# Kernel optimization log

Hardware: AMD Instinct MI355X
Metric: run time of the kernel (lower is better)

Reference implementation:

```python
import jax, jax.numpy as jnp
import numpy as np

TOP_K = 4  # num_experts_per_tok


def setup_inputs() -> dict:
    key = jax.random.key(0)
    ks = jax.random.split(key, 5)
    T, H, M, E = 2048, 1024, 512, 32
    sH = 1.0 / np.sqrt(H)
    sM = 1.0 / np.sqrt(M)
    return {
        "x": jax.random.normal(ks[0], (T, 1, H), dtype=jnp.float32),
        "gate_w": jax.random.normal(ks[1], (E, H), dtype=jnp.float32) * sH,   # router nn.Linear weight [E, H]
        "w_gate": jax.random.normal(ks[2], (E, M, H), dtype=jnp.float32) * sH,  # ffn_gate_exps, per expert [M, H]
        "w_up": jax.random.normal(ks[3], (E, M, H), dtype=jnp.float32) * sH,    # ffn_up_exps
        "w_down": jax.random.normal(ks[4], (E, H, M), dtype=jnp.float32) * sM,  # ffn_down_exps, per expert [H, M]
    }


def reference(x, gate_w, w_gate, w_up, w_down):
    # x: [T, S, H]; only the last position is used (decode path)
    curr = x[:, -1, :]                                   # [T, H]
    T = curr.shape[0]
    E = gate_w.shape[0]

    # router: logits = curr @ gate_w^T, top-k, softmax over top-k logits
    logits = curr @ gate_w.T                             # [T, E]
    topk_vals, topk_ids = jax.lax.top_k(logits, TOP_K)   # [T, K]
    topk_weights = jax.nn.softmax(topk_vals, axis=-1)    # [T, K]

    # dense routing matrix [T, E]: weight for chosen experts, 0 elsewhere
    route = jnp.zeros((T, E), dtype=curr.dtype)
    route = route.at[jnp.arange(T)[:, None], topk_ids].add(topk_weights)

    # expert MLPs: gate/up -> silu(gate)*up -> down, weighted combine
    gate_act = jnp.einsum('th,emh->tem', curr, w_gate)   # [T, E, M]
    up_act = jnp.einsum('th,emh->tem', curr, w_up)
    mixed = jax.nn.silu(gate_act) * up_act * route[:, :, None]
    out = jnp.einsum('tem,ehm->th', mixed, w_down)       # [T, H]

    return out.reshape(T, 1, -1)
```

## Files before the change

kernel.cpp:

```cpp
#include <hip/hip_runtime.h>
#include <math.h>

#define T_TOK 2048
#define H_DIM 1024
#define M_DIM 512
#define E_NUM 32
#define TOPK  4

#define BT  128
#define BK  32
#define GU_BM 64
#define DN_BH 128
#define MAX_TILES 96

typedef __bf16 bf16x8 __attribute__((ext_vector_type(8)));
typedef float f32x4 __attribute__((ext_vector_type(4)));
typedef unsigned short u16x8 __attribute__((ext_vector_type(8)));

__device__ __forceinline__ unsigned short f2bf(float f) {
  unsigned u = __float_as_uint(f);
  return (unsigned short)((u + 0x7fffu + ((u >> 16) & 1u)) >> 16);
}
__device__ __forceinline__ float bf2f(unsigned short h) {
  return __uint_as_float(((unsigned)h) << 16);
}
__device__ __forceinline__ f32x4 mfma16(bf16x8 a, bf16x8 b, f32x4 c) {
  return __builtin_amdgcn_mfma_f32_16x16x32_bf16(a, b, c, 0, 0, 0);
}

__global__ __launch_bounds__(512) void split_x_kernel(
    const float* __restrict__ x, unsigned short* __restrict__ xh,
    unsigned short* __restrict__ xl) {
  int i = (blockIdx.x * 512 + threadIdx.x) * 8;
  float t8[8];
  *(float4*)t8 = *(const float4*)(x + i);
  *(float4*)(t8 + 4) = *(const float4*)(x + i + 4);
  u16x8 hv, lv;
  #pragma unroll
  for (int j = 0; j < 8; ++j) {
    unsigned short h = f2bf(t8[j]);
    hv[j] = h;
    lv[j] = f2bf(t8[j] - bf2f(h));
  }
  *(u16x8*)(xh + i) = hv;
  *(u16x8*)(xl + i) = lv;
}

__global__ __launch_bounds__(256) void gating_kernel(
    const float* __restrict__ x, const float* __restrict__ gate_w,
    int* __restrict__ topk_ids, float* __restrict__ topk_w) {
  __shared__ float xr[H_DIM];
  __shared__ float logits[E_NUM];
  int t = blockIdx.x;
  int tid = threadIdx.x;
  const float* xrow = x + (size_t)t * H_DIM;
  *(float4*)(xr + tid * 4) = *(const float4*)(xrow + tid * 4);
  __syncthreads();
  int wave = tid >> 6, lane = tid & 63;
  const float4* x4 = (const float4*)xr;
  for (int e8 = 0; e8 < 8; ++e8) {
    int e = wave * 8 + e8;
    const float4* g4 = (const float4*)(gate_w + (size_t)e * H_DIM);
    float p = 0.f;
    #pragma unroll
    for (int i = 0; i < 4; ++i) {
      float4 a = x4[lane + i * 64];
      float4 b = g4[lane + i * 64];
      p += a.x * b.x + a.y * b.y + a.z * b.z + a.w * b.w;
    }
    for (int off = 32; off > 0; off >>= 1) p += __shfl_down(p, off, 64);
    if (lane == 0) logits[e] = p;
  }
  __syncthreads();
  if (tid == 0) {
    float v[E_NUM];
    for (int e = 0; e < E_NUM; ++e) v[e] = logits[e];
    int ids[TOPK]; float vals[TOPK];
    for (int k = 0; k < TOPK; ++k) {
      int bi = 0; float bv = -1e30f;
      for (int e = 0; e < E_NUM; ++e) if (v[e] > bv) { bv = v[e]; bi = e; }
      ids[k] = bi; vals[k] = bv; v[bi] = -1e30f;
    }
    float m = vals[0];
    float w[TOPK]; float s = 0.f;
    for (int k = 0; k < TOPK; ++k) { w[k] = expf(vals[k] - m); s += w[k]; }
    float inv = 1.f / s;
    for (int k = 0; k < TOPK; ++k) {
      topk_ids[t * TOPK + k] = ids[k];
      topk_w[t * TOPK + k]   = w[k] * inv;
    }
  }
}

__global__ __launch_bounds__(256) void scatter_kernel(
    const int* __restrict__ topk_ids, int* __restrict__ cursors,
    int* __restrict__ tok_list) {
  int g = blockIdx.x * 256 + threadIdx.x;
  if (g >= T_TOK * TOPK) return;
  int e = topk_ids[g];
  int slot = atomicAdd(&cursors[e], 1);
  tok_list[e * T_TOK + slot] = g;
}

__global__ void build_tiles(const int* __restrict__ cursors,
                            int* __restrict__ n_tiles, int* __restrict__ tile_list) {
  int lane = threadIdx.x;
  int nt = 0;
  if (lane < E_NUM) nt = (cursors[lane] + BT - 1) / BT;
  int pfx = nt;
  for (int off = 1; off < 64; off <<= 1) {
    int v = __shfl_up(pfx, off, 64);
    if (lane >= off) pfx += v;
  }
  int excl = pfx - nt;
  if (lane == E_NUM - 1) *n_tiles = pfx;
  if (lane < E_NUM)
    for (int i = 0; i < nt; ++i) tile_list[excl + i] = (lane << 8) | i;
}

__global__ __launch_bounds__(512) void gateup_mfma(
    const unsigned short* __restrict__ xh, const unsigned short* __restrict__ xl,
    const float* __restrict__ w_gate, const float* __restrict__ w_up,
    const float* __restrict__ topk_w,
    const int* __restrict__ cursors, const int* __restrict__ tok_list,
    const int* __restrict__ n_tiles, const int* __restrict__ tile_list,
    unsigned short* __restrict__ mixed) {
  if (blockIdx.y >= *n_tiles) return;
  int tid = threadIdx.x;
  int entry = tile_list[blockIdx.y];
  int e = entry >> 8, tile = entry & 255;
  int cnt = cursors[e];
  int m0 = blockIdx.x * GU_BM;

  __shared__ unsigned short Ah[BT * BK], Al[BT * BK];
  __shared__ unsigned short Gh[GU_BM * BK], Uh[GU_BM * BK];
  __shared__ int   ent[BT];
  __shared__ float rw[BT];

  if (tid < BT) {
    int idx = tile * BT + tid;
    int en = (idx < cnt) ? tok_list[e * T_TOK + idx] : -1;
    ent[tid] = en;
    rw[tid]  = (en >= 0) ? topk_w[en] : 0.f;
  }
  __syncthreads();

  int arow = tid >> 2, akq = tid & 3;
  int aen = ent[arow];
  if (aen < 0) aen = ent[0];
  const unsigned short* pAh = xh + (size_t)(aen >> 2) * H_DIM + akq * 8;
  const unsigned short* pAl = xl + (size_t)(aen >> 2) * H_DIM + akq * 8;
  int aoff = (arow >> 4) * 512 + akq * 128 + (arow & 15) * 8;

  int bslot = tid & 255;
  int brow = bslot >> 2, bkq = bslot & 3;
  const float* pB = ((tid < 256) ? w_gate : w_up) +
                    ((size_t)e * M_DIM + m0 + brow) * H_DIM + bkq * 8;
  unsigned short* Bdst = (tid < 256) ? Gh : Uh;
  int boff = (brow >> 4) * 512 + bkq * 128 + (brow & 15) * 8;

  int lane = tid & 63, wid = tid >> 6;
  int wr = (wid >> 1) * 32;
  int wc = (wid & 1) * 32;
  int l16 = lane * 8;

  f32x4 accg[2][2] = {}; f32x4 accu[2][2] = {};

  u16x8 rah, ral; float bf8[8];
  rah = *(const u16x8*)pAh;
  ral = *(const u16x8*)pAl;
  *(float4*)bf8 = *(const float4*)pB;
  *(float4*)(bf8 + 4) = *(const float4*)(pB + 4);

  const int NK = H_DIM / BK;
  for (int ks = 0; ks < NK; ++ks) {
    u16x8 bh;
    #pragma unroll
    for (int j = 0; j < 8; ++j) bh[j] = f2bf(bf8[j]);
    __syncthreads();
    *(u16x8*)&Ah[aoff] = rah;
    *(u16x8*)&Al[aoff] = ral;
    *(u16x8*)&Bdst[boff] = bh;
    __syncthreads();
    if (ks + 1 < NK) {
      int kq = (ks + 1) * BK;
      rah = *(const u16x8*)(pAh + kq);
      ral = *(const u16x8*)(pAl + kq);
      *(float4*)bf8 = *(const float4*)(pB + kq);
      *(float4*)(bf8 + 4) = *(const float4*)(pB + kq + 4);
    }
    int ab = (wr >> 4) * 512 + l16;
    bf16x8 a0h = *(const bf16x8*)&Ah[ab];
    bf16x8 a1h = *(const bf16x8*)&Ah[ab + 512];
    bf16x8 a0l = *(const bf16x8*)&Al[ab];
    bf16x8 a1l = *(const bf16x8*)&Al[ab + 512];
    #pragma unroll
    for (int nf = 0; nf < 2; ++nf) {
      int nb = ((wc >> 4) + nf) * 512 + l16;
      bf16x8 g = *(const bf16x8*)&Gh[nb];
      bf16x8 u = *(const bf16x8*)&Uh[nb];
      accg[0][nf] = mfma16(a0h, g, accg[0][nf]);
      accg[0][nf] = mfma16(a0l, g, accg[0][nf]);
      accg[1][nf] = mfma16(a1h, g, accg[1][nf]);
      accg[1][nf] = mfma16(a1l, g, accg[1][nf]);
      accu[0][nf] = mfma16(a0h, u, accu[0][nf]);
      accu[0][nf] = mfma16(a0l, u, accu[0][nf]);
      accu[1][nf] = mfma16(a1h, u, accu[1][nf]);
      accu[1][nf] = mfma16(a1l, u, accu[1][nf]);
    }
  }

  #pragma unroll
  for (int mf = 0; mf < 2; ++mf) {
    #pragma unroll
    for (int j = 0; j < 4; ++j) {
      int tr = wr + mf * 16 + (lane >> 4) * 4 + j;
      int en = ent[tr];
      if (en < 0) continue;
      float w = rw[tr];
      #pragma unroll
      for (int nf = 0; nf < 2; ++nf) {
        float g = accg[mf][nf][j], u = accu[mf][nf][j];
        float val = (g / (1.f + __expf(-g))) * u * w;
        mixed[(size_t)en * M_DIM + m0 + wc + nf * 16 + (lane & 15)] = f2bf(val);
      }
    }
  }
}

__global__ __launch_bounds__(512) void down_mfma(
    const float* __restrict__ w_down, const unsigned short* __restrict__ mixed,
    const int* __restrict__ cursors, const int* __restrict__ tok_list,
    const int* __restrict__ n_tiles, const int* __restrict__ tile_list,
    float* __restrict__ out) {
  if (blockIdx.y >= *n_tiles) return;
  int tid = threadIdx.x;
  int entry = tile_list[blockIdx.y];
  int e = entry >> 8, tile = entry & 255;
  int cnt = cursors[e];
  int h0 = blockIdx.x * DN_BH;

  __shared__ unsigned short As[BT * BK];
  __shared__ unsigned short Bs[DN_BH * BK];
  __shared__ int ent[BT];

  if (tid < BT) {
    int idx = tile * BT + tid;
    ent[tid] = (idx < cnt) ? tok_list[e * T_TOK + idx] : -1;
  }
  __syncthreads();

  int arow = tid >> 2, akq = tid & 3;
  int aen = ent[arow];
  if (aen < 0) aen = ent[0];
  const unsigned short* pA = mixed + (size_t)aen * M_DIM + akq * 8;
  int aoff = (arow >> 4) * 512 + akq * 128 + (arow & 15) * 8;

  const float* pB = w_down + ((size_t)e * H_DIM + h0 + arow) * M_DIM + akq * 8;

  int lane = tid & 63, wid = tid >> 6;
  int wr = (wid >> 1) * 32, wc = (wid & 1) * 64;
  int l16 = lane * 8;

  f32x4 acc[2][4] = {};
  u16x8 ra; float bf8[8];
  ra = *(const u16x8*)pA;
  *(float4*)bf8 = *(const float4*)pB;
  *(float4*)(bf8 + 4) = *(const float4*)(pB + 4);

  const int NK = M_DIM / BK;
  for (int ks = 0; ks < NK; ++ks) {
    u16x8 bh;
    #pragma unroll
    for (int j = 0; j < 8; ++j) bh[j] = f2bf(bf8[j]);
    __syncthreads();
    *(u16x8*)&As[aoff] = ra;
    *(u16x8*)&Bs[aoff] = bh;
    __syncthreads();
    if (ks + 1 < NK) {
      int kq = (ks + 1) * BK;
      ra = *(const u16x8*)(pA + kq);
      *(float4*)bf8 = *(const float4*)(pB + kq);
      *(float4*)(bf8 + 4) = *(const float4*)(pB + kq + 4);
    }
    int ab = (wr >> 4) * 512 + l16;
    bf16x8 a0 = *(const bf16x8*)&As[ab];
    bf16x8 a1 = *(const bf16x8*)&As[ab + 512];
    #pragma unroll
    for (int nf = 0; nf < 4; ++nf) {
      bf16x8 b = *(const bf16x8*)&Bs[((wc >> 4) + nf) * 512 + l16];
      acc[0][nf] = mfma16(a0, b, acc[0][nf]);
      acc[1][nf] = mfma16(a1, b, acc[1][nf]);
    }
  }

  #pragma unroll
  for (int mf = 0; mf < 2; ++mf) {
    #pragma unroll
    for (int j = 0; j < 4; ++j) {
      int tr = wr + mf * 16 + (lane >> 4) * 4 + j;
      int en = ent[tr];
      if (en < 0) continue;
      int t = en >> 2;
      #pragma unroll
      for (int nf = 0; nf < 4; ++nf)
        atomicAdd(&out[(size_t)t * H_DIM + h0 + wc + nf * 16 + (lane & 15)],
                  acc[mf][nf][j]);
    }
  }
}

extern "C" void kernel_launch(void* const* d_in, const int* in_sizes, int n_in,
                              void* d_out, int out_size, void* d_ws, size_t ws_size,
                              hipStream_t stream) {
  const float* x      = (const float*)d_in[0];
  const float* gate_w = (const float*)d_in[1];
  const float* w_gate = (const float*)d_in[2];
  const float* w_up   = (const float*)d_in[3];
  const float* w_down = (const float*)d_in[4];
  float* out = (float*)d_out;

  char* ws = (char*)d_ws;
  size_t off = 0;
  int*   topk_ids  = (int*)(ws + off);   off += (size_t)T_TOK * TOPK * 4;
  float* topk_w    = (float*)(ws + off); off += (size_t)T_TOK * TOPK * 4;
  int*   cursors   = (int*)(ws + off);   off += 256;
  int*   n_tiles   = (int*)(ws + off);   off += 64;
  int*   tile_list = (int*)(ws + off);   off += MAX_TILES * 4 + 64;
  int*   tok_list  = (int*)(ws + off);   off += (size_t)E_NUM * T_TOK * 4;
  unsigned short* x_hi  = (unsigned short*)(ws + off); off += (size_t)T_TOK * H_DIM * 2;
  unsigned short* x_lo  = (unsigned short*)(ws + off); off += (size_t)T_TOK * H_DIM * 2;
  unsigned short* mixed = (unsigned short*)(ws + off); off += (size_t)T_TOK * TOPK * M_DIM * 2;

  hipMemsetAsync(cursors, 0, E_NUM * sizeof(int), stream);
  hipMemsetAsync(out, 0, (size_t)T_TOK * H_DIM * sizeof(float), stream);

  split_x_kernel<<<T_TOK * H_DIM / (512 * 8), 512, 0, stream>>>(x, x_hi, x_lo);
  gating_kernel<<<T_TOK, 256, 0, stream>>>(x, gate_w, topk_ids, topk_w);
  scatter_kernel<<<(T_TOK * TOPK) / 256, 256, 0, stream>>>(topk_ids, cursors, tok_list);
  build_tiles<<<1, 64, 0, stream>>>(cursors, n_tiles, tile_list);
  gateup_mfma<<<dim3(M_DIM / GU_BM, MAX_TILES), 512, 0, stream>>>(
      x_hi, x_lo, w_gate, w_up, topk_w, cursors, tok_list, n_tiles, tile_list, mixed);
  down_mfma<<<dim3(H_DIM / DN_BH, MAX_TILES), 512, 0, stream>>>(
      w_down, mixed, cursors, tok_list, n_tiles, tile_list, out);
}
```

Before: 163.1 us.

## Fuse split/scatter into gating, use global_load_lds with fp32 B tiles and smaller token tiles

After: 212.8 us. 30.4% more time.

```diff
diff --git a/kernel.cpp b/kernel.cpp
--- a/kernel.cpp
+++ b/kernel.cpp
@@ -7,15 +7,15 @@
 #define E_NUM 32
 #define TOPK  4
 
-#define BT  128
-#define BK  32
+#define BT    64
+#define BK    32
 #define GU_BM 64
 #define DN_BH 128
-#define MAX_TILES 96
+#define MAX_TILES 160
 
 typedef __bf16 bf16x8 __attribute__((ext_vector_type(8)));
 typedef float f32x4 __attribute__((ext_vector_type(4)));
-typedef unsigned short u16x8 __attribute__((ext_vector_type(8)));
+typedef unsigned short u16x4 __attribute__((ext_vector_type(4)));
 
 __device__ __forceinline__ unsigned short f2bf(float f) {
   unsigned u = __float_as_uint(f);
@@ -27,34 +27,42 @@
 __device__ __forceinline__ f32x4 mfma16(bf16x8 a, bf16x8 b, f32x4 c) {
   return __builtin_amdgcn_mfma_f32_16x16x32_bf16(a, b, c, 0, 0, 0);
 }
-
-__global__ __launch_bounds__(512) void split_x_kernel(
-    const float* __restrict__ x, unsigned short* __restrict__ xh,
-    unsigned short* __restrict__ xl) {
-  int i = (blockIdx.x * 512 + threadIdx.x) * 8;
-  float t8[8];
-  *(float4*)t8 = *(const float4*)(x + i);
-  *(float4*)(t8 + 4) = *(const float4*)(x + i + 4);
-  u16x8 hv, lv;
+__device__ __forceinline__ void gload16(const void* g, void* l) {
+  __builtin_amdgcn_global_load_lds(
+      (const __attribute__((address_space(1))) unsigned int*)g,
+      (__attribute__((address_space(3))) unsigned int*)l, 16, 0, 0);
+}
+__device__ __forceinline__ bf16x8 cvt8(f32x4 a, f32x4 b) {
+  bf16x8 r;
   #pragma unroll
-  for (int j = 0; j < 8; ++j) {
-    unsigned short h = f2bf(t8[j]);
-    hv[j] = h;
-    lv[j] = f2bf(t8[j] - bf2f(h));
-  }
-  *(u16x8*)(xh + i) = hv;
-  *(u16x8*)(xl + i) = lv;
+  for (int j = 0; j < 4; ++j) { r[j] = (__bf16)a[j]; r[4 + j] = (__bf16)b[j]; }
+  return r;
 }
 
 __global__ __launch_bounds__(256) void gating_kernel(
     const float* __restrict__ x, const float* __restrict__ gate_w,
-    int* __restrict__ topk_ids, float* __restrict__ topk_w) {
+    unsigned short* __restrict__ xh, unsigned short* __restrict__ xl,
+    float* __restrict__ topk_w, int* __restrict__ cursors,
+    int* __restrict__ tok_list) {
   __shared__ float xr[H_DIM];
   __shared__ float logits[E_NUM];
   int t = blockIdx.x;
   int tid = threadIdx.x;
   const float* xrow = x + (size_t)t * H_DIM;
-  *(float4*)(xr + tid * 4) = *(const float4*)(xrow + tid * 4);
+  float4 v = *(const float4*)(xrow + tid * 4);
+  *(float4*)(xr + tid * 4) = v;
+  {
+    float f[4] = {v.x, v.y, v.z, v.w};
+    u16x4 hv, lv;
+    #pragma unroll
+    for (int j = 0; j < 4; ++j) {
+      unsigned short h = f2bf(f[j]);
+      hv[j] = h;
+      lv[j] = f2bf(f[j] - bf2f(h));
+    }
+    *(u16x4*)(xh + (size_t)t * H_DIM + tid * 4) = hv;
+    *(u16x4*)(xl + (size_t)t * H_DIM + tid * 4) = lv;
+  }
   __syncthreads();
   int wave = tid >> 6, lane = tid & 63;
   const float4* x4 = (const float4*)xr;
@@ -73,33 +81,25 @@
   }
   __syncthreads();
   if (tid == 0) {
-    float v[E_NUM];
-    for (int e = 0; e < E_NUM; ++e) v[e] = logits[e];
+    float vv[E_NUM];
+    for (int e = 0; e < E_NUM; ++e) vv[e] = logits[e];
     int ids[TOPK]; float vals[TOPK];
     for (int k = 0; k < TOPK; ++k) {
       int bi = 0; float bv = -1e30f;
-      for (int e = 0; e < E_NUM; ++e) if (v[e] > bv) { bv = v[e]; bi = e; }
-      ids[k] = bi; vals[k] = bv; v[bi] = -1e30f;
+      for (int e = 0; e < E_NUM; ++e) if (vv[e] > bv) { bv = vv[e]; bi = e; }
+      ids[k] = bi; vals[k] = bv; vv[bi] = -1e30f;
     }
     float m = vals[0];
     float w[TOPK]; float s = 0.f;
     for (int k = 0; k < TOPK; ++k) { w[k] = expf(vals[k] - m); s += w[k]; }
     float inv = 1.f / s;
     for (int k = 0; k < TOPK; ++k) {
-      topk_ids[t * TOPK + k] = ids[k];
-      topk_w[t * TOPK + k]   = w[k] * inv;
-    }
-  }
-}
-
-__global__ __launch_bounds__(256) void scatter_kernel(
-    const int* __restrict__ topk_ids, int* __restrict__ cursors,
-    int* __restrict__ tok_list) {
-  int g = blockIdx.x * 256 + threadIdx.x;
-  if (g >= T_TOK * TOPK) return;
-  int e = topk_ids[g];
-  int slot = atomicAdd(&cursors[e], 1);
-  tok_list[e * T_TOK + slot] = g;
+      int g = t * TOPK + k;
+      topk_w[g] = w[k] * inv;
+      int slot = atomicAdd(&cursors[ids[k]], 1);
+      tok_list[ids[k] * T_TOK + slot] = g;
+    }
+  }
 }
 
 __global__ void build_tiles(const int* __restrict__ cursors,
@@ -118,7 +118,7 @@
     for (int i = 0; i < nt; ++i) tile_list[excl + i] = (lane << 8) | i;
 }
 
-__global__ __launch_bounds__(512) void gateup_mfma(
+__global__ __launch_bounds__(256, 6) void gateup_mfma(
     const unsigned short* __restrict__ xh, const unsigned short* __restrict__ xl,
     const float* __restrict__ w_gate, const float* __restrict__ w_up,
     const float* __restrict__ topk_w,
@@ -132,8 +132,10 @@
   int cnt = cursors[e];
   int m0 = blockIdx.x * GU_BM;
 
-  __shared__ unsigned short Ah[BT * BK], Al[BT * BK];
-  __shared__ unsigned short Gh[GU_BM * BK], Uh[GU_BM * BK];
+  __shared__ unsigned short Ah[BT * BK];
+  __shared__ unsigned short Al[BT * BK];
+  __shared__ float Gs[GU_BM * BK];
+  __shared__ float Us[GU_BM * BK];
   __shared__ int   ent[BT];
   __shared__ float rw[BT];
 
@@ -145,60 +147,52 @@
   }
   __syncthreads();
 
-  int arow = tid >> 2, akq = tid & 3;
-  int aen = ent[arow];
-  if (aen < 0) aen = ent[0];
-  const unsigned short* pAh = xh + (size_t)(aen >> 2) * H_DIM + akq * 8;
-  const unsigned short* pAl = xl + (size_t)(aen >> 2) * H_DIM + akq * 8;
-  int aoff = (arow >> 4) * 512 + akq * 128 + (arow & 15) * 8;
-
-  int bslot = tid & 255;
-  int brow = bslot >> 2, bkq = bslot & 3;
-  const float* pB = ((tid < 256) ? w_gate : w_up) +
-                    ((size_t)e * M_DIM + m0 + brow) * H_DIM + bkq * 8;
-  unsigned short* Bdst = (tid < 256) ? Gh : Uh;
-  int boff = (brow >> 4) * 512 + bkq * 128 + (brow & 15) * 8;
+  int arow = ((tid >> 6) << 4) + (tid & 15);
+  int askq = (tid >> 4) & 3;
+  int aen = ent[arow]; if (aen < 0) aen = ent[0];
+  const unsigned short* gAh = xh + (size_t)(aen >> 2) * H_DIM + askq * 8;
+  const unsigned short* gAl = xl + (size_t)(aen >> 2) * H_DIM + askq * 8;
+  unsigned short* lAh = &Ah[tid * 8];
+  unsigned short* lAl = &Al[tid * 8];
+
+  int c0 = tid, c1 = tid + 256;
+  int br0 = ((c0 >> 7) << 4) + ((c0 >> 1) & 15), bk0 = ((c0 >> 5) & 3) * 8 + (c0 & 1) * 4;
+  int br1 = ((c1 >> 7) << 4) + ((c1 >> 1) & 15), bk1 = ((c1 >> 5) & 3) * 8 + (c1 & 1) * 4;
+  const float* gG0 = w_gate + ((size_t)e * M_DIM + m0 + br0) * H_DIM + bk0;
+  const float* gG1 = w_gate + ((size_t)e * M_DIM + m0 + br1) * H_DIM + bk1;
+  const float* gU0 = w_up   + ((size_t)e * M_DIM + m0 + br0) * H_DIM + bk0;
+  const float* gU1 = w_up   + ((size_t)e * M_DIM + m0 + br1) * H_DIM + bk1;
+  float* lG0 = &Gs[c0 * 4]; float* lG1 = &Gs[c1 * 4];
+  float* lU0 = &Us[c0 * 4]; float* lU1 = &Us[c1 * 4];
 
   int lane = tid & 63, wid = tid >> 6;
   int wr = (wid >> 1) * 32;
   int wc = (wid & 1) * 32;
-  int l16 = lane * 8;
+  int l8 = lane * 8;
 
   f32x4 accg[2][2] = {}; f32x4 accu[2][2] = {};
-
-  u16x8 rah, ral; float bf8[8];
-  rah = *(const u16x8*)pAh;
-  ral = *(const u16x8*)pAl;
-  *(float4*)bf8 = *(const float4*)pB;
-  *(float4*)(bf8 + 4) = *(const float4*)(pB + 4);
 
   const int NK = H_DIM / BK;
   for (int ks = 0; ks < NK; ++ks) {
-    u16x8 bh;
-    #pragma unroll
-    for (int j = 0; j < 8; ++j) bh[j] = f2bf(bf8[j]);
+    int ka = ks * BK;
+    gload16(gAh + ka, lAh);
+    gload16(gAl + ka, lAl);
+    gload16(gG0 + ka, lG0);
+    gload16(gG1 + ka, lG1);
+    gload16(gU0 + ka, lU0);
+    gload16(gU1 + ka, lU1);
     __syncthreads();
-    *(u16x8*)&Ah[aoff] = rah;
-    *(u16x8*)&Al[aoff] = ral;
-    *(u16x8*)&Bdst[boff] = bh;
-    __syncthreads();
-    if (ks + 1 < NK) {
-      int kq = (ks + 1) * BK;
-      rah = *(const u16x8*)(pAh + kq);
-      ral = *(const u16x8*)(pAl + kq);
-      *(float4*)bf8 = *(const float4*)(pB + kq);
-      *(float4*)(bf8 + 4) = *(const float4*)(pB + kq + 4);
-    }
-    int ab = (wr >> 4) * 512 + l16;
+
+    int ab = (wr >> 4) * 512 + l8;
     bf16x8 a0h = *(const bf16x8*)&Ah[ab];
     bf16x8 a1h = *(const bf16x8*)&Ah[ab + 512];
     bf16x8 a0l = *(const bf16x8*)&Al[ab];
     bf16x8 a1l = *(const bf16x8*)&Al[ab + 512];
     #pragma unroll
     for (int nf = 0; nf < 2; ++nf) {
-      int nb = ((wc >> 4) + nf) * 512 + l16;
-      bf16x8 g = *(const bf16x8*)&Gh[nb];
-      bf16x8 u = *(const bf16x8*)&Uh[nb];
+      int nb = ((wc >> 4) + nf) * 512 + l8;
+      bf16x8 g = cvt8(*(const f32x4*)&Gs[nb], *(const f32x4*)&Gs[nb + 4]);
+      bf16x8 u = cvt8(*(const f32x4*)&Us[nb], *(const f32x4*)&Us[nb + 4]);
       accg[0][nf] = mfma16(a0h, g, accg[0][nf]);
       accg[0][nf] = mfma16(a0l, g, accg[0][nf]);
       accg[1][nf] = mfma16(a1h, g, accg[1][nf]);
@@ -208,6 +202,7 @@
       accu[1][nf] = mfma16(a1h, u, accu[1][nf]);
       accu[1][nf] = mfma16(a1l, u, accu[1][nf]);
     }
+    __syncthreads();
   }
 
   #pragma unroll
@@ -222,13 +217,15 @@
       for (int nf = 0; nf < 2; ++nf) {
         float g = accg[mf][nf][j], u = accu[mf][nf][j];
         float val = (g / (1.f + __expf(-g))) * u * w;
-        mixed[(size_t)en * M_DIM + m0 + wc + nf * 16 + (lane & 15)] = f2bf(val);
+        __bf16 bv = (__bf16)val;
+        mixed[(size_t)en * M_DIM + m0 + wc + nf * 16 + (lane & 15)] =
+            *(unsigned short*)&bv;
       }
     }
   }
 }
 
-__global__ __launch_bounds__(512) void down_mfma(
+__global__ __launch_bounds__(256, 7) void down_mfma(
     const float* __restrict__ w_down, const unsigned short* __restrict__ mixed,
     const int* __restrict__ cursors, const int* __restrict__ tok_list,
     const int* __restrict__ n_tiles, const int* __restrict__ tile_list,
@@ -241,7 +238,7 @@
   int h0 = blockIdx.x * DN_BH;
 
   __shared__ unsigned short As[BT * BK];
-  __shared__ unsigned short Bs[DN_BH * BK];
+  __shared__ float Bs[DN_BH * BK];
   __shared__ int ent[BT];
 
   if (tid < BT) {
@@ -250,48 +247,51 @@
   }
   __syncthreads();
 
-  int arow = tid >> 2, akq = tid & 3;
-  int aen = ent[arow];
-  if (aen < 0) aen = ent[0];
-  const unsigned short* pA = mixed + (size_t)aen * M_DIM + akq * 8;
-  int aoff = (arow >> 4) * 512 + akq * 128 + (arow & 15) * 8;
-
-  const float* pB = w_down + ((size_t)e * H_DIM + h0 + arow) * M_DIM + akq * 8;
+  int arow = ((tid >> 6) << 4) + (tid & 15);
+  int askq = (tid >> 4) & 3;
+  int aen = ent[arow]; if (aen < 0) aen = ent[0];
+  const unsigned short* gA = mixed + (size_t)aen * M_DIM + askq * 8;
+  unsigned short* lA = &As[tid * 8];
+
+  const float* gB[4];
+  float* lB[4];
+  #pragma unroll
+  for (int i = 0; i < 4; ++i) {
+    int c = tid + 256 * i;
+    int row = ((c >> 7) << 4) + ((c >> 1) & 15);
+    int kof = ((c >> 5) & 3) * 8 + (c & 1) * 4;
+    gB[i] = w_down + ((size_t)e * H_DIM + h0 + row) * M_DIM + kof;
+    lB[i] = &Bs[c * 4];
+  }
 
   int lane = tid & 63, wid = tid >> 6;
-  int wr = (wid >> 1) * 32, wc = (wid & 1) * 64;
-  int l16 = lane * 8;
+  int wr = (wid >> 1) * 32;
+  int wc = (wid & 1) * 64;
+  int l8 = lane * 8;
 
   f32x4 acc[2][4] = {};
-  u16x8 ra; float bf8[8];
-  ra = *(const u16x8*)pA;
-  *(float4*)bf8 = *(const float4*)pB;
-  *(float4*)(bf8 + 4) = *(const float4*)(pB + 4);
 
   const int NK = M_DIM / BK;
   for (int ks = 0; ks < NK; ++ks) {
-    u16x8 bh;
-    #pragma unroll
-    for (int j = 0; j < 8; ++j) bh[j] = f2bf(bf8[j]);
+    int ka = ks * BK;
+    gload16(gA + ka, lA);
+    gload16(gB[0] + ka, lB[0]);
+    gload16(gB[1] + ka, lB[1]);
+    gload16(gB[2] + ka, lB[2]);
+    gload16(gB[3] + ka, lB[3]);
     __syncthreads();
-    *(u16x8*)&As[aoff] = ra;
-    *(u16x8*)&Bs[aoff] = bh;
-    __syncthreads();
-    if (ks + 1 < NK) {
-      int kq = (ks + 1) * BK;
-      ra = *(const u16x8*)(pA + kq);
-      *(float4*)bf8 = *(const float4*)(pB + kq);
-      *(float4*)(bf8 + 4) = *(const float4*)(pB + kq + 4);
-    }
-    int ab = (wr >> 4) * 512 + l16;
+
+    int ab = (wr >> 4) * 512 + l8;
     bf16x8 a0 = *(const bf16x8*)&As[ab];
     bf16x8 a1 = *(const bf16x8*)&As[ab + 512];
     #pragma unroll
     for (int nf = 0; nf < 4; ++nf) {
-      bf16x8 b = *(const bf16x8*)&Bs[((wc >> 4) + nf) * 512 + l16];
+      int nb = ((wc >> 4) + nf) * 512 + l8;
+      bf16x8 b = cvt8(*(const f32x4*)&Bs[nb], *(const f32x4*)&Bs[nb + 4]);
       acc[0][nf] = mfma16(a0, b, acc[0][nf]);
       acc[1][nf] = mfma16(a1, b, acc[1][nf]);
     }
+    __syncthreads();
   }
 
   #pragma unroll
@@ -322,7 +322,6 @@
 
   char* ws = (char*)d_ws;
   size_t off = 0;
-  int*   topk_ids  = (int*)(ws + off);   off += (size_t)T_TOK * TOPK * 4;
   float* topk_w    = (float*)(ws + off); off += (size_t)T_TOK * TOPK * 4;
   int*   cursors   = (int*)(ws + off);   off += 256;
   int*   n_tiles   = (int*)(ws + off);   off += 64;
@@ -335,12 +334,11 @@
   hipMemsetAsync(cursors, 0, E_NUM * sizeof(int), stream);
   hipMemsetAsync(out, 0, (size_t)T_TOK * H_DIM * sizeof(float), stream);
 
-  split_x_kernel<<<T_TOK * H_DIM / (512 * 8), 512, 0, stream>>>(x, x_hi, x_lo);
-  gating_kernel<<<T_TOK, 256, 0, stream>>>(x, gate_w, topk_ids, topk_w);
-  scatter_kernel<<<(T_TOK * TOPK) / 256, 256, 0, stream>>>(topk_ids, cursors, tok_list);
+  gating_kernel<<<T_TOK, 256, 0, stream>>>(x, gate_w, x_hi, x_lo, topk_w,
+                                           cursors, tok_list);
   build_tiles<<<1, 64, 0, stream>>>(cursors, n_tiles, tile_list);
-  gateup_mfma<<<dim3(M_DIM / GU_BM, MAX_TILES), 512, 0, stream>>>(
+  gateup_mfma<<<dim3(M_DIM / GU_BM, MAX_TILES), 256, 0, stream>>>(
       x_hi, x_lo, w_gate, w_up, topk_w, cursors, tok_list, n_tiles, tile_list, mixed);
-  down_mfma<<<dim3(H_DIM / DN_BH, MAX_TILES), 512, 0, stream>>>(
+  down_mfma<<<dim3(H_DIM / DN_BH, MAX_TILES), 256, 0, stream>>>(
       w_down, mixed, cursors, tok_list, n_tiles, tile_list, out);
 }
```
